# Kernel tuning notes

Hardware: AMD Instinct MI355X
Metric: run time of the kernel (lower is better)

The kernel has to match this reference:

```python
import jax, jax.numpy as jnp
import numpy as np

N = 6144      # nodes
DIN = 65      # input_dim (1 time + 64 space coords)
DOUT = 65     # output_dim per head
H = 4         # nheads
EPS = 1e-7
MIN = 1e-15
# curvature c = 1 throughout (MultiHeadGraphAttentionLayer hardcodes curvature=1)

def arcosh(z):
    return jnp.log(z + jnp.sqrt(jnp.maximum(z * z - 1.0, 0.0)))

def hyp_proj(u):
    # project onto hyperboloid: recompute time coord
    y = u[..., 1:]
    t = jnp.sqrt(1.0 + jnp.sum(y * y, -1, keepdims=True))
    return jnp.concatenate([t, y], -1)

def expmap0(u):
    v = u[..., 1:]
    n = jnp.maximum(jnp.linalg.norm(v, axis=-1, keepdims=True), MIN)
    return jnp.concatenate([jnp.cosh(n), jnp.sinh(n) * v / n], -1)

def logmap0(x):
    y = x[..., 1:]
    n = jnp.maximum(jnp.linalg.norm(y, axis=-1, keepdims=True), MIN)
    t = jnp.maximum(x[..., :1], 1.0 + EPS)
    return jnp.concatenate([jnp.zeros_like(t), arcosh(t) * y / n], -1)

def hyp_linear(x, W):
    # HypLinear (use_bias=False, eval mode): mobius_matvec = exp0(log0(x) @ W^T), then proj
    return hyp_proj(expmap0(logmap0(x) @ W.T))

def to_poincare(x):
    return x[..., 1:] / (x[..., :1] + 1.0)

def to_hyperboloid(p):
    s = jnp.sum(p * p, -1, keepdims=True)
    return jnp.concatenate([1.0 + s, 2.0 * p], -1) / jnp.maximum(1.0 - s, MIN)

def mobius_half(v):
    # 0.5 (x) v  (mobius scalar multiplication, c=1)
    n = jnp.maximum(jnp.linalg.norm(v, axis=-1, keepdims=True), MIN)
    return jnp.tanh(0.5 * jnp.arctanh(jnp.minimum(n, 1.0 - EPS))) * v / n

def head(x, adj_t, Wa, Wd, Wo):
    att = hyp_linear(x, Wa)   # [N, DOUT]
    red = hyp_linear(x, Wd)   # [N, DOUT]
    # pairwise hyperboloid sqdist via Minkowski inner product (negate time coord)
    am = att.at[:, 0].multiply(-1.0)
    theta = jnp.maximum(-(am @ att.T), 1.0 + EPS)          # [N, N]
    S = jnp.minimum(arcosh(theta) ** 2, 50.0)
    # coef[i, j] = -adj[j, i] * sqdist for incoming edges (mask = adj^T)
    coef = jnp.where(adj_t > 0.01, -adj_t * S, 0.0)
    # F.normalize along incoming-edge axis (zeros don't change the L2 norm)
    a = coef / jnp.maximum(jnp.linalg.norm(coef, axis=-1, keepdims=True), 1e-12)
    pv = to_poincare(red)                                   # [N, DOUT-1]
    lam = 2.0 / jnp.maximum(1.0 - jnp.sum(pv * pv, -1), MIN)  # conformal factors [N]
    num = (a * lam[None, :]) @ pv                           # [N, DOUT-1]
    den = jnp.sum(jnp.abs(a) * (lam - 1.0)[None, :], -1, keepdims=True)
    m = mobius_half(num / jnp.maximum(den, MIN))            # mobius midpoint
    return hyp_linear(to_hyperboloid(m), Wo)                # [N, DOUT]

def reference(x, adj, W_att, W_data, W_out, W_lin):
    adj_t = adj.T
    hs = jnp.stack([head(x, adj_t, W_att[h], W_data[h], W_out[h]) for h in range(H)], axis=1)  # [N, H, DOUT]
    p = to_poincare(hs).reshape(x.shape[0], -1)             # PoincareBall.concat -> [N, H*(DOUT-1)]
    return hyp_linear(to_hyperboloid(p), W_lin)             # [N, H*DOUT]

def setup_inputs():
    key = jax.random.key(0)
    ks = jax.random.split(key, 8)
    sp = 0.1 * jax.random.normal(ks[0], (N, DIN - 1), jnp.float32)
    x = jnp.concatenate([jnp.sqrt(1.0 + jnp.sum(sp * sp, -1, keepdims=True)), sp], -1)
    adj = (jax.random.uniform(ks[1], (N, N)) < 32.0 / N).astype(jnp.float32)
    adj = jnp.maximum(adj, jnp.eye(N, dtype=jnp.float32))  # every node >=1 incoming edge
    def xavier(k, shape):
        b = (6.0 / (shape[0] + shape[1])) ** 0.5
        return jax.random.uniform(k, shape, jnp.float32, -b, b)
    W_att = jnp.stack([xavier(jax.random.fold_in(ks[2], h), (DOUT, DIN)) for h in range(H)])
    W_data = jnp.stack([xavier(jax.random.fold_in(ks[3], h), (DOUT, DIN)) for h in range(H)])
    W_out = jnp.stack([xavier(jax.random.fold_in(ks[4], h), (DOUT, DOUT)) for h in range(H)])
    W_lin = xavier(ks[5], (H * DOUT, H * (DOUT - 1) + 1))
    return {"x": x, "adj": adj, "W_att": W_att, "W_data": W_data, "W_out": W_out, "W_lin": W_lin}
```

## Files before the change

### kernel.cpp

```cpp
#include <hip/hip_runtime.h>
#include <hip/hip_fp16.h>
#include <math.h>

#define N 6144
#define H 4
#define CAP 128
#define MINF 1e-15f
#define ONE_EPS  1.0000001192092896f
#define ONE_MEPS 0.9999998807907104f

__device__ __forceinline__ float wave_reduce_sum(float v) {
    v += __shfl_xor(v, 32, 64);
    v += __shfl_xor(v, 16, 64);
    v += __shfl_xor(v, 8, 64);
    v += __shfl_xor(v, 4, 64);
    v += __shfl_xor(v, 2, 64);
    v += __shfl_xor(v, 1, 64);
    return v;
}

__device__ __forceinline__ float arcosh_f(float z) {
    return logf(z + sqrtf(fmaxf(z * z - 1.0f, 0.0f)));
}

__device__ __forceinline__ void h8_to_f(float4 r, float* o) {
    __half2* h = (__half2*)&r;
    #pragma unroll
    for (int q = 0; q < 4; q++) {
        float2 f = __half22float2(h[q]);
        o[2 * q + 0] = f.x;
        o[2 * q + 1] = f.y;
    }
}

__device__ __forceinline__ int bitrev4(int t) {
    return ((t & 1) << 3) | ((t & 2) << 1) | ((t & 4) >> 1) | ((t & 8) >> 3);
}

__global__ void k_prep(const float* __restrict__ x, float* __restrict__ lmv,
                       const float* __restrict__ W_att, const float* __restrict__ W_data,
                       const float* __restrict__ W_out, const float* __restrict__ Wl,
                       float* __restrict__ Bp, float* __restrict__ Bo,
                       float* __restrict__ WlT, int* __restrict__ cnt) {
    int b = blockIdx.x;
    if (b < 1536) {
        int i = b * 4 + (threadIdx.x >> 6);
        int lane = threadIdx.x & 63;
        float y = x[i * 65 + 1 + lane];
        float ss = wave_reduce_sum(y * y);
        float n = fmaxf(sqrtf(ss), MINF);
        float t = fmaxf(x[i * 65], ONE_EPS);
        lmv[i * 64 + lane] = arcosh_f(t) * y / n;
    } else if (b < 1728) {
        int tid = (b - 1536) * 256 + threadIdx.x;
        int m = tid >> 12;
        int r = tid & 4095;
        int k = r >> 6, o = r & 63;
        const float* src;
        if (m < 4) src = W_att + m * 65 * 65;
        else if (m < 8) src = W_data + (m - 4) * 65 * 65;
        else src = W_out + (m - 8) * 65 * 65;
        if (m < 8) {
            Bp[m * 4096 + k * 64 + o] = src[(1 + o) * 65 + (1 + k)];
        } else {
            int dk = (k & 3) * 16 + bitrev4(k >> 2);
            Bo[(m - 8) * 4096 + k * 64 + o] = src[(1 + o) * 65 + (1 + dk)];
        }
    } else if (b < 1808) {
        int L = ((b - 1728) * 256 + threadIdx.x) * 4;
        int k = L / 320, o0 = L % 320;
        float v[4];
        #pragma unroll
        for (int q = 0; q < 4; q++) {
            int o = o0 + q;
            v[q] = (o < 259) ? Wl[(size_t)(1 + o) * 257 + 1 + k] : 0.f;
        }
        *(float4*)(WlT + L) = make_float4(v[0], v[1], v[2], v[3]);
    } else {
        cnt[(b - 1808) * 256 + threadIdx.x] = 0;
    }
}

__global__ void __launch_bounds__(256) k_csr_gemm(
        const float* __restrict__ adj, int* __restrict__ cnt, int* __restrict__ idx,
        const float* __restrict__ lmv, const float* __restrict__ Bp,
        __half* __restrict__ kv, float2* __restrict__ a0l) {
    __shared__ float smem[64 * 65];
    if (blockIdx.x < 768) {
        float (*As)[64] = (float(*)[64])smem;
        float (*Bs)[64] = (float(*)[64])(smem + 1024);
        float (*Cs)[65] = (float(*)[65])smem;
        int my = blockIdx.x / 96;
        int ix = blockIdx.x % 96;
        const float* Bb = Bp + (size_t)my * 4096;
        int i0 = ix * 64;
        int tid = threadIdx.x;
        int tx = tid & 15, ty = tid >> 4;
        float acc[4][4] = {};
        for (int k0 = 0; k0 < 64; k0 += 16) {
            {
                int mm = tid >> 2, kq = tid & 3;
                float4 v = *(const float4*)(lmv + (size_t)(i0 + mm) * 64 + k0 + kq * 4);
                As[kq * 4 + 0][mm] = v.x;
                As[kq * 4 + 1][mm] = v.y;
                As[kq * 4 + 2][mm] = v.z;
                As[kq * 4 + 3][mm] = v.w;
            }
            {
                int kk = tid >> 4, o4 = tid & 15;
                float4 bvv = *(const float4*)(Bb + (k0 + kk) * 64 + o4 * 4);
                *(float4*)&Bs[kk][o4 * 4] = bvv;
            }
            __syncthreads();
            #pragma unroll
            for (int kk = 0; kk < 16; kk++) {
                float4 av = *(const float4*)&As[kk][ty * 4];
                float4 bv = *(const float4*)&Bs[kk][tx * 4];
                float a[4] = {av.x, av.y, av.z, av.w};
                float b[4] = {bv.x, bv.y, bv.z, bv.w};
                #pragma unroll
                for (int r = 0; r < 4; r++)
                    #pragma unroll
                    for (int c = 0; c < 4; c++) acc[r][c] += a[r] * b[c];
            }
            __syncthreads();
        }
        #pragma unroll
        for (int r = 0; r < 4; r++)
            #pragma unroll
            for (int c = 0; c < 4; c++)
                Cs[ty * 4 + r][tx * 4 + c] = acc[r][c];
        __syncthreads();
        int w = tid >> 6, lane = tid & 63;
        bool isAtt = my < 4;
        int h = my & 3;
        #pragma unroll 1
        for (int r = 0; r < 16; r++) {
            int row = w * 16 + r;
            int i = i0 + row;
            float u = Cs[row][lane];
            float nn = fmaxf(sqrtf(wave_reduce_sum(u * u)), MINF);
            if (isAtt) {
                float sha = sinhf(nn);
                kv[((size_t)h * N + i) * 128 + lane] = __float2half(sha * u / nn);
                if (lane == 0) a0l[h * N + i].x = coshf(nn);
            } else {
                float shd = sinhf(nn), chd = coshf(nn);
                float pvd = (shd * u / nn) / (chd + 1.0f);
                kv[((size_t)h * N + i) * 128 + 64 + lane] = __float2half(pvd);
                float sp = wave_reduce_sum(pvd * pvd);
                if (lane == 0) a0l[h * N + i].y = 2.0f / fmaxf(1.0f - sp, MINF);
            }
        }
    } else {
        const float4* a4 = (const float4*)adj;
        const unsigned STRIDE = 1048576u;
        unsigned e0 = (blockIdx.x - 768) * 256 + threadIdx.x;
        float4 v0 = a4[e0];
        float4 v1 = a4[e0 + STRIDE];
        #pragma unroll 1
        for (int it = 0; it < 9; it++) {
            float4 vn;
            if (it < 7) vn = a4[e0 + (unsigned)(it + 2) * STRIDE];
            unsigned base = (e0 + (unsigned)it * STRIDE) * 4u;
            float vals[4] = {v0.x, v0.y, v0.z, v0.w};
            #pragma unroll
            for (int q = 0; q < 4; q++) {
                if (vals[q] > 0.01f) {
                    unsigned t = base + q;
                    int j = t / N;
                    int i = t % N;
                    int pos = atomicAdd(&cnt[i], 1);
                    if (pos < CAP) idx[i * CAP + pos] = j;
                }
            }
            v0 = v1;
            v1 = vn;
        }
    }
}

__global__ void __launch_bounds__(256) k_attn(
        const int* __restrict__ cnt, const int* __restrict__ idx,
        const __half* __restrict__ kv, const float2* __restrict__ a0l,
        float* __restrict__ lm2) {
    int w = threadIdx.x >> 6, lane = threadIdx.x & 63;
    int gb = blockIdx.x;
    int slot = gb & 7;
    int h = slot >> 1;
    int iblk = (gb >> 3) * 2 + (slot & 1);
    int i = iblk * 4 + w;

    const __half* kvh = kv + (size_t)h * N * 128;
    const float2* a0lh = a0l + (size_t)h * N;
    int c = lane & 3, t = lane >> 2;

    float ai[16];
    {
        float4 r0 = *(const float4*)(kvh + (size_t)i * 128 + c * 16);
        float4 r1 = *(const float4*)(kvh + (size_t)i * 128 + c * 16 + 8);
        h8_to_f(r0, ai);
        h8_to_f(r1, ai + 8);
    }
    float ai0 = a0lh[i].x;
    int nn = min(cnt[i], CAP);

    float accd = 0.f, accss = 0.f;
    float accn16[16] = {};
    for (int base = 0; base < nn; base += 16) {
        int tt = base + t;
        bool act = tt < nn;
        int j = act ? idx[i * CAP + tt] : i;
        float2 al = a0lh[j];
        const __half* row = kvh + (size_t)j * 128;
        float4 b0 = *(const float4*)(row + c * 16);
        float4 b1 = *(const float4*)(row + c * 16 + 8);
        float4 p0 = *(const float4*)(row + 64 + c * 16);
        float4 p1 = *(const float4*)(row + 64 + c * 16 + 8);
        float bv[16], pw[16];
        h8_to_f(b0, bv);
        h8_to_f(b1, bv + 8);
        h8_to_f(p0, pw);
        h8_to_f(p1, pw + 8);
        float d = 0.f;
        #pragma unroll
        for (int k = 0; k < 16; k++) d += ai[k] * bv[k];
        d += __shfl_xor(d, 1, 64);
        d += __shfl_xor(d, 2, 64);
        float theta = fmaxf(ai0 * al.x - d, ONE_EPS);
        float ar = arcosh_f(theta);
        float S = fminf(ar * ar, 50.0f);
        if (!act || j == i) S = 0.f;
        float wq = S * al.y;
        if (c == 0) {
            accd += S * (al.y - 1.0f);
            accss += S * S;
        }
        #pragma unroll
        for (int k = 0; k < 16; k++) accn16[k] = fmaf(wq, pw[k], accn16[k]);
    }
    accd = wave_reduce_sum(accd);
    accss = wave_reduce_sum(accss);
    float nrm = fmaxf(sqrtf(accss), 1e-12f);
    float den = fmaxf(accd / nrm, MINF);
    float scl = 1.0f / (nrm * den);

    float r8[8];
    {
        bool b0 = t & 1;
        #pragma unroll
        for (int kk = 0; kk < 8; kk++) {
            float mine = b0 ? accn16[kk + 8] : accn16[kk];
            float send = b0 ? accn16[kk] : accn16[kk + 8];
            r8[kk] = mine + __shfl_xor(send, 4, 64);
        }
    }
    float r4[4];
    {
        bool b1 = t & 2;
        #pragma unroll
        for (int kk = 0; kk < 4; kk++) {
            float mine = b1 ? r8[kk + 4] : r8[kk];
            float send = b1 ? r8[kk] : r8[kk + 4];
            r4[kk] = mine + __shfl_xor(send, 8, 64);
        }
    }
    float r2[2];
    {
        bool b2 = t & 4;
        #pragma unroll
        for (int kk = 0; kk < 2; kk++) {
            float mine = b2 ? r4[kk + 2] : r4[kk];
            float send = b2 ? r4[kk] : r4[kk + 2];
            r2[kk] = mine + __shfl_xor(send, 16, 64);
        }
    }
    float r1;
    {
        bool b3 = t & 8;
        float mine = b3 ? r2[1] : r2[0];
        float send = b3 ? r2[0] : r2[1];
        r1 = mine + __shfl_xor(send, 32, 64);
    }

    float v = -scl * r1;
    float nv = fmaxf(sqrtf(wave_reduce_sum(v * v)), MINF);
    float nc = fminf(nv, ONE_MEPS);
    float mh = tanhf(0.5f * atanhf(nc));
    float md = mh * v / nv;
    float s = wave_reduce_sum(md * md);
    float Dh = fmaxf(1.0f - s, MINF);
    float hb0 = (1.0f + s) / Dh;
    float hbv = 2.0f * md / Dh;
    float nh = fmaxf(2.0f * sqrtf(s) / Dh, MINF);
    float t2 = fmaxf(hb0, ONE_EPS);
    lm2[((size_t)h * N + i) * 64 + lane] = arcosh_f(t2) * hbv / nh;
}

#define PS 272
#define BS5 336
__global__ void __launch_bounds__(256) k_tail(
        const float* __restrict__ lm2, const float* __restrict__ Bo,
        const float* __restrict__ WlT, float* __restrict__ out) {
    __shared__ float smem[5376 + 16 * PS];
    float* As1 = smem;
    float* Bs1 = smem + 1088;
    float* Bs5 = smem;
    float* P   = smem + 5376;

    int i0 = blockIdx.x * 16;
    int tid = threadIdx.x;
    int ty = tid >> 4;
    int tx = tid & 15;

    for (int h = 0; h < H; h++) {
        {
            float4 v = *(const float4*)(lm2 + ((size_t)h * N + i0 + ty) * 64 + tx * 4);
            *(float4*)(As1 + ty * 68 + tx * 4) = v;
        }
        float acc[4] = {0.f, 0.f, 0.f, 0.f};
        for (int k0 = 0; k0 < 64; k0 += 16) {
            {
                *(float4*)(Bs1 + ty * 64 + tx * 4) =
                    *(const float4*)(Bo + (size_t)h * 4096 + (k0 + ty) * 64 + tx * 4);
            }
            __syncthreads();
            #pragma unroll
            for (int kk = 0; kk < 16; kk++) {
                float a = As1[ty * 68 + k0 + kk];
                float4 bv = *(const float4*)(Bs1 + kk * 64 + tx * 4);
                acc[0] += a * bv.x;
                acc[1] += a * bv.y;
                acc[2] += a * bv.z;
                acc[3] += a * bv.w;
            }
            __syncthreads();
        }
        float ss = acc[0] * acc[0] + acc[1] * acc[1] + acc[2] * acc[2] + acc[3] * acc[3];
        ss += __shfl_xor(ss, 1, 64);
        ss += __shfl_xor(ss, 2, 64);
        ss += __shfl_xor(ss, 4, 64);
        ss += __shfl_xor(ss, 8, 64);
        float nn = fmaxf(sqrtf(ss), MINF);
        float sh = sinhf(nn), ch = coshf(nn);
        float* Pr = P + ty * PS + h * 64 + tx * 4;
        Pr[0] = (sh * acc[0] / nn) / (ch + 1.0f);
        Pr[1] = (sh * acc[1] / nn) / (ch + 1.0f);
        Pr[2] = (sh * acc[2] / nn) / (ch + 1.0f);
        Pr[3] = (sh * acc[3] / nn) / (ch + 1.0f);
    }
    __syncthreads();

    {
        float sp = 0.f;
        float4 pl[4];
        #pragma unroll
        for (int q = 0; q < 4; q++) {
            pl[q] = *(const float4*)(P + ty * PS + q * 64 + tx * 4);
            sp += pl[q].x * pl[q].x + pl[q].y * pl[q].y
                + pl[q].z * pl[q].z + pl[q].w * pl[q].w;
        }
        sp += __shfl_xor(sp, 1, 64);
        sp += __shfl_xor(sp, 2, 64);
        sp += __shfl_xor(sp, 4, 64);
        sp += __shfl_xor(sp, 8, 64);
        float Dh = fmaxf(1.0f - sp, MINF);
        float t2 = fmaxf((1.0f + sp) / Dh, ONE_EPS);
        float nh = fmaxf(2.0f * sqrtf(sp) / Dh, MINF);
        float ar2 = arcosh_f(t2);
        #pragma unroll
        for (int q = 0; q < 4; q++) {
            float4 v = pl[q];
            v.x = ar2 * (2.0f * v.x / Dh) / nh;
            v.y = ar2 * (2.0f * v.y / Dh) / nh;
            v.z = ar2 * (2.0f * v.z / Dh) / nh;
            v.w = ar2 * (2.0f * v.w / Dh) / nh;
            *(float4*)(P + ty * PS + q * 64 + tx * 4) = v;
        }
    }
    __syncthreads();

    float acc2[5][4] = {};
    for (int k0 = 0; k0 < 256; k0 += 16) {
        {
            #pragma unroll
            for (int q = 0; q < 5; q++)
                *(float4*)(Bs5 + ty * BS5 + q * 64 + tx * 4) =
                    *(const float4*)(WlT + (size_t)(k0 + ty) * 320 + q * 64 + tx * 4);
        }
        __syncthreads();
        #pragma unroll
        for (int kq = 0; kq < 4; kq++) {
            float4 pv4 = *(const float4*)(P + ty * PS + k0 + kq * 4);
            float av[4] = {pv4.x, pv4.y, pv4.z, pv4.w};
            #pragma unroll
            for (int j = 0; j < 4; j++) {
                float a = av[j];
                int kk = kq * 4 + j;
                #pragma unroll
                for (int q = 0; q < 5; q++) {
                    float4 bv = *(const float4*)(Bs5 + kk * BS5 + q * 64 + tx * 4);
                    acc2[q][0] += a * bv.x;
                    acc2[q][1] += a * bv.y;
                    acc2[q][2] += a * bv.z;
                    acc2[q][3] += a * bv.w;
                }
            }
        }
        __syncthreads();
    }

    float ss2 = 0.f;
    #pragma unroll
    for (int q = 0; q < 5; q++)
        ss2 += acc2[q][0] * acc2[q][0] + acc2[q][1] * acc2[q][1]
             + acc2[q][2] * acc2[q][2] + acc2[q][3] * acc2[q][3];
    ss2 += __shfl_xor(ss2, 1, 64);
    ss2 += __shfl_xor(ss2, 2, 64);
    ss2 += __shfl_xor(ss2, 4, 64);
    ss2 += __shfl_xor(ss2, 8, 64);
    float nv = fmaxf(sqrtf(ss2), MINF);
    float sh2 = sinhf(nv);
    float scale = sh2 / nv;
    size_t ob = (size_t)(i0 + ty) * 260;
    #pragma unroll
    for (int q = 0; q < 4; q++) {
        int o = q * 64 + tx * 4;
        out[ob + 1 + o + 0] = scale * acc2[q][0];
        out[ob + 1 + o + 1] = scale * acc2[q][1];
        out[ob + 1 + o + 2] = scale * acc2[q][2];
        out[ob + 1 + o + 3] = scale * acc2[q][3];
    }
    if (tx == 0) {
        out[ob] = sqrtf(1.0f + sh2 * sh2);
        out[ob + 257] = scale * acc2[4][0];
        out[ob + 258] = scale * acc2[4][1];
        out[ob + 259] = scale * acc2[4][2];
    }
}

extern "C" void kernel_launch(void* const* d_in, const int* in_sizes, int n_in,
                              void* d_out, int out_size, void* d_ws, size_t ws_size,
                              hipStream_t stream) {
    const float* x = (const float*)d_in[0];
    const float* adj = (const float*)d_in[1];
    const float* W_att = (const float*)d_in[2];
    const float* W_data = (const float*)d_in[3];
    const float* W_out = (const float*)d_in[4];
    const float* W_lin = (const float*)d_in[5];
    float* out = (float*)d_out;

    char* ws = (char*)d_ws;
    size_t off = 0;
    auto alloc = [&](size_t bytes) {
        void* ptr = ws + off;
        off += (bytes + 255) & ~(size_t)255;
        return ptr;
    };
    int* cnt = (int*)alloc((size_t)N * 4);
    int* idx = (int*)alloc((size_t)N * CAP * 4);
    float* lmv = (float*)alloc((size_t)N * 64 * 4);
    __half* kv = (__half*)alloc((size_t)H * N * 128 * 2);
    float2* a0l = (float2*)alloc((size_t)H * N * 8);
    float* lm2 = (float*)alloc((size_t)H * N * 64 * 4);
    float* Bp = (float*)alloc((size_t)8 * 4096 * 4);
    float* Bo = (float*)alloc((size_t)4 * 4096 * 4);
    float* WlT = (float*)alloc((size_t)256 * 320 * 4);

    k_prep<<<1832, 256, 0, stream>>>(x, lmv, W_att, W_data, W_out, W_lin,
                                     Bp, Bo, WlT, cnt);
    k_csr_gemm<<<4864, 256, 0, stream>>>(adj, cnt, idx, lmv, Bp, kv, a0l);
    k_attn<<<6144, 256, 0, stream>>>(cnt, idx, kv, a0l, lm2);
    k_tail<<<N / 16, 256, 0, stream>>>(lm2, Bo, WlT, out);
}
```

Before: 313.9 us.

## Fuse all stages into one cooperative persistent kernel with grid syncs

```diff
diff --git a/kernel.cpp b/kernel.cpp
--- a/kernel.cpp
+++ b/kernel.cpp
@@ -1,6 +1,9 @@
 #include <hip/hip_runtime.h>
 #include <hip/hip_fp16.h>
+#include <hip/hip_cooperative_groups.h>
 #include <math.h>
+
+namespace cg = cooperative_groups;
 
 #define N 6144
 #define H 4
@@ -8,6 +11,7 @@
 #define MINF 1e-15f
 #define ONE_EPS  1.0000001192092896f
 #define ONE_MEPS 0.9999998807907104f
+#define NBLK 1024
 
 __device__ __forceinline__ float wave_reduce_sum(float v) {
     v += __shfl_xor(v, 32, 64);
@@ -37,24 +41,26 @@
     return ((t & 1) << 3) | ((t & 2) << 1) | ((t & 4) >> 1) | ((t & 8) >> 3);
 }
 
-__global__ void k_prep(const float* __restrict__ x, float* __restrict__ lmv,
-                       const float* __restrict__ W_att, const float* __restrict__ W_data,
-                       const float* __restrict__ W_out, const float* __restrict__ Wl,
-                       float* __restrict__ Bp, float* __restrict__ Bo,
-                       float* __restrict__ WlT, int* __restrict__ cnt) {
-    int b = blockIdx.x;
+
+__device__ __forceinline__ void prep_unit(
+        int b, int tid,
+        const float* __restrict__ x, float* __restrict__ lmv,
+        const float* __restrict__ W_att, const float* __restrict__ W_data,
+        const float* __restrict__ W_out, const float* __restrict__ Wl,
+        float* __restrict__ Bp, float* __restrict__ Bo,
+        float* __restrict__ WlT, int* __restrict__ cnt) {
     if (b < 1536) {
-        int i = b * 4 + (threadIdx.x >> 6);
-        int lane = threadIdx.x & 63;
+        int i = b * 4 + (tid >> 6);
+        int lane = tid & 63;
         float y = x[i * 65 + 1 + lane];
         float ss = wave_reduce_sum(y * y);
         float n = fmaxf(sqrtf(ss), MINF);
         float t = fmaxf(x[i * 65], ONE_EPS);
         lmv[i * 64 + lane] = arcosh_f(t) * y / n;
     } else if (b < 1728) {
-        int tid = (b - 1536) * 256 + threadIdx.x;
-        int m = tid >> 12;
-        int r = tid & 4095;
+        int t = (b - 1536) * 256 + tid;
+        int m = t >> 12;
+        int r = t & 4095;
         int k = r >> 6, o = r & 63;
         const float* src;
         if (m < 4) src = W_att + m * 65 * 65;
@@ -67,7 +73,7 @@
             Bo[(m - 8) * 4096 + k * 64 + o] = src[(1 + o) * 65 + (1 + dk)];
         }
     } else if (b < 1808) {
-        int L = ((b - 1728) * 256 + threadIdx.x) * 4;
+        int L = ((b - 1728) * 256 + tid) * 4;
         int k = L / 320, o0 = L % 320;
         float v[4];
         #pragma unroll
@@ -77,120 +83,108 @@
         }
         *(float4*)(WlT + L) = make_float4(v[0], v[1], v[2], v[3]);
     } else {
-        cnt[(b - 1808) * 256 + threadIdx.x] = 0;
-    }
-}
-
-__global__ void __launch_bounds__(256) k_csr_gemm(
-        const float* __restrict__ adj, int* __restrict__ cnt, int* __restrict__ idx,
+        cnt[(b - 1808) * 256 + tid] = 0;
+    }
+}
+
+__device__ __forceinline__ void scan_adj(
+        const float4* __restrict__ a4, int* __restrict__ cnt,
+        int* __restrict__ idx, unsigned e0, unsigned stride, int iters) {
+    float4 v0 = a4[e0];
+    #pragma unroll 1
+    for (int it = 0; it < iters; it++) {
+        float4 vn;
+        if (it + 1 < iters) vn = a4[e0 + (unsigned)(it + 1) * stride];
+        unsigned base = (e0 + (unsigned)it * stride) * 4u;
+        float vals[4] = {v0.x, v0.y, v0.z, v0.w};
+        #pragma unroll
+        for (int q = 0; q < 4; q++) {
+            if (vals[q] > 0.01f) {
+                unsigned t = base + q;
+                int j = t / N;
+                int i = t % N;
+                int pos = atomicAdd(&cnt[i], 1);
+                if (pos < CAP) idx[i * CAP + pos] = j;
+            }
+        }
+        v0 = vn;
+    }
+}
+
+__device__ __forceinline__ void gemm1_tile(
+        int my, int ix, int tid, float* smem,
         const float* __restrict__ lmv, const float* __restrict__ Bp,
         __half* __restrict__ kv, float2* __restrict__ a0l) {
-    __shared__ float smem[64 * 65];
-    if (blockIdx.x < 768) {
-        float (*As)[64] = (float(*)[64])smem;
-        float (*Bs)[64] = (float(*)[64])(smem + 1024);
-        float (*Cs)[65] = (float(*)[65])smem;
-        int my = blockIdx.x / 96;
-        int ix = blockIdx.x % 96;
-        const float* Bb = Bp + (size_t)my * 4096;
-        int i0 = ix * 64;
-        int tid = threadIdx.x;
-        int tx = tid & 15, ty = tid >> 4;
-        float acc[4][4] = {};
-        for (int k0 = 0; k0 < 64; k0 += 16) {
-            {
-                int mm = tid >> 2, kq = tid & 3;
-                float4 v = *(const float4*)(lmv + (size_t)(i0 + mm) * 64 + k0 + kq * 4);
-                As[kq * 4 + 0][mm] = v.x;
-                As[kq * 4 + 1][mm] = v.y;
-                As[kq * 4 + 2][mm] = v.z;
-                As[kq * 4 + 3][mm] = v.w;
-            }
-            {
-                int kk = tid >> 4, o4 = tid & 15;
-                float4 bvv = *(const float4*)(Bb + (k0 + kk) * 64 + o4 * 4);
-                *(float4*)&Bs[kk][o4 * 4] = bvv;
-            }
-            __syncthreads();
+    float (*As)[64] = (float(*)[64])smem;
+    float (*Bs)[64] = (float(*)[64])(smem + 1024);
+    float (*Cs)[65] = (float(*)[65])smem;
+    const float* Bb = Bp + (size_t)my * 4096;
+    int i0 = ix * 64;
+    int tx = tid & 15, ty = tid >> 4;
+    float acc[4][4] = {};
+    for (int k0 = 0; k0 < 64; k0 += 16) {
+        {
+            int mm = tid >> 2, kq = tid & 3;
+            float4 v = *(const float4*)(lmv + (size_t)(i0 + mm) * 64 + k0 + kq * 4);
+            As[kq * 4 + 0][mm] = v.x;
+            As[kq * 4 + 1][mm] = v.y;
+            As[kq * 4 + 2][mm] = v.z;
+            As[kq * 4 + 3][mm] = v.w;
+        }
+        {
+            int kk = tid >> 4, o4 = tid & 15;
+            float4 bvv = *(const float4*)(Bb + (k0 + kk) * 64 + o4 * 4);
+            *(float4*)&Bs[kk][o4 * 4] = bvv;
+        }
+        __syncthreads();
+        #pragma unroll
+        for (int kk = 0; kk < 16; kk++) {
+            float4 av = *(const float4*)&As[kk][ty * 4];
+            float4 bv = *(const float4*)&Bs[kk][tx * 4];
+            float a[4] = {av.x, av.y, av.z, av.w};
+            float b[4] = {bv.x, bv.y, bv.z, bv.w};
             #pragma unroll
-            for (int kk = 0; kk < 16; kk++) {
-                float4 av = *(const float4*)&As[kk][ty * 4];
-                float4 bv = *(const float4*)&Bs[kk][tx * 4];
-                float a[4] = {av.x, av.y, av.z, av.w};
-                float b[4] = {bv.x, bv.y, bv.z, bv.w};
+            for (int r = 0; r < 4; r++)
                 #pragma unroll
-                for (int r = 0; r < 4; r++)
-                    #pragma unroll
-                    for (int c = 0; c < 4; c++) acc[r][c] += a[r] * b[c];
-            }
-            __syncthreads();
-        }
-        #pragma unroll
-        for (int r = 0; r < 4; r++)
-            #pragma unroll
-            for (int c = 0; c < 4; c++)
-                Cs[ty * 4 + r][tx * 4 + c] = acc[r][c];
+                for (int c = 0; c < 4; c++) acc[r][c] += a[r] * b[c];
+        }
         __syncthreads();
-        int w = tid >> 6, lane = tid & 63;
-        bool isAtt = my < 4;
-        int h = my & 3;
-        #pragma unroll 1
-        for (int r = 0; r < 16; r++) {
-            int row = w * 16 + r;
-            int i = i0 + row;
-            float u = Cs[row][lane];
-            float nn = fmaxf(sqrtf(wave_reduce_sum(u * u)), MINF);
-            if (isAtt) {
-                float sha = sinhf(nn);
-                kv[((size_t)h * N + i) * 128 + lane] = __float2half(sha * u / nn);
-                if (lane == 0) a0l[h * N + i].x = coshf(nn);
-            } else {
-                float shd = sinhf(nn), chd = coshf(nn);
-                float pvd = (shd * u / nn) / (chd + 1.0f);
-                kv[((size_t)h * N + i) * 128 + 64 + lane] = __float2half(pvd);
-                float sp = wave_reduce_sum(pvd * pvd);
-                if (lane == 0) a0l[h * N + i].y = 2.0f / fmaxf(1.0f - sp, MINF);
-            }
-        }
-    } else {
-        const float4* a4 = (const float4*)adj;
-        const unsigned STRIDE = 1048576u;
-        unsigned e0 = (blockIdx.x - 768) * 256 + threadIdx.x;
-        float4 v0 = a4[e0];
-        float4 v1 = a4[e0 + STRIDE];
-        #pragma unroll 1
-        for (int it = 0; it < 9; it++) {
-            float4 vn;
-            if (it < 7) vn = a4[e0 + (unsigned)(it + 2) * STRIDE];
-            unsigned base = (e0 + (unsigned)it * STRIDE) * 4u;
-            float vals[4] = {v0.x, v0.y, v0.z, v0.w};
-            #pragma unroll
-            for (int q = 0; q < 4; q++) {
-                if (vals[q] > 0.01f) {
-                    unsigned t = base + q;
-                    int j = t / N;
-                    int i = t % N;
-                    int pos = atomicAdd(&cnt[i], 1);
-                    if (pos < CAP) idx[i * CAP + pos] = j;
-                }
-            }
-            v0 = v1;
-            v1 = vn;
-        }
-    }
-}
-
-__global__ void __launch_bounds__(256) k_attn(
+    }
+    #pragma unroll
+    for (int r = 0; r < 4; r++)
+        #pragma unroll
+        for (int c = 0; c < 4; c++)
+            Cs[ty * 4 + r][tx * 4 + c] = acc[r][c];
+    __syncthreads();
+    int w = tid >> 6, lane = tid & 63;
+    bool isAtt = my < 4;
+    int h = my & 3;
+    #pragma unroll 1
+    for (int r = 0; r < 16; r++) {
+        int row = w * 16 + r;
+        int i = i0 + row;
+        float u = Cs[row][lane];
+        float nn = fmaxf(sqrtf(wave_reduce_sum(u * u)), MINF);
+        if (isAtt) {
+            float sha = sinhf(nn);
+            kv[((size_t)h * N + i) * 128 + lane] = __float2half(sha * u / nn);
+            if (lane == 0) a0l[h * N + i].x = coshf(nn);
+        } else {
+            float shd = sinhf(nn), chd = coshf(nn);
+            float pvd = (shd * u / nn) / (chd + 1.0f);
+            kv[((size_t)h * N + i) * 128 + 64 + lane] = __float2half(pvd);
+            float sp = wave_reduce_sum(pvd * pvd);
+            if (lane == 0) a0l[h * N + i].y = 2.0f / fmaxf(1.0f - sp, MINF);
+        }
+    }
+    __syncthreads();
+}
+
+__device__ __forceinline__ void attn_unit(
+        int i, int h, int lane,
         const int* __restrict__ cnt, const int* __restrict__ idx,
         const __half* __restrict__ kv, const float2* __restrict__ a0l,
         float* __restrict__ lm2) {
-    int w = threadIdx.x >> 6, lane = threadIdx.x & 63;
-    int gb = blockIdx.x;
-    int slot = gb & 7;
-    int h = slot >> 1;
-    int iblk = (gb >> 3) * 2 + (slot & 1);
-    int i = iblk * 4 + w;
-
     const __half* kvh = kv + (size_t)h * N * 128;
     const float2* a0lh = a0l + (size_t)h * N;
     int c = lane & 3, t = lane >> 2;
@@ -299,17 +293,14 @@
 
 #define PS 272
 #define BS5 336
-__global__ void __launch_bounds__(256) k_tail(
+__device__ __forceinline__ void tail_tile(
+        int i0, int tid, float* smem,
         const float* __restrict__ lm2, const float* __restrict__ Bo,
         const float* __restrict__ WlT, float* __restrict__ out) {
-    __shared__ float smem[5376 + 16 * PS];
     float* As1 = smem;
     float* Bs1 = smem + 1088;
     float* Bs5 = smem;
     float* P   = smem + 5376;
-
-    int i0 = blockIdx.x * 16;
-    int tid = threadIdx.x;
     int ty = tid >> 4;
     int tx = tid & 15;
 
@@ -439,6 +430,91 @@
     }
 }
 
+__global__ void __launch_bounds__(256, 4) k_mega(
+        const float* __restrict__ x, const float* __restrict__ adj,
+        const float* __restrict__ W_att, const float* __restrict__ W_data,
+        const float* __restrict__ W_out, const float* __restrict__ Wl,
+        float* __restrict__ lmv, float* __restrict__ Bp, float* __restrict__ Bo,
+        float* __restrict__ WlT, int* __restrict__ cnt, int* __restrict__ idx,
+        __half* __restrict__ kv, float2* __restrict__ a0l,
+        float* __restrict__ lm2, float* __restrict__ out) {
+    cg::grid_group grid = cg::this_grid();
+    __shared__ float smem[9728];
+    int bid = blockIdx.x, tid = threadIdx.x;
+
+    for (int u = bid; u < 1832; u += NBLK)
+        prep_unit(u, tid, x, lmv, W_att, W_data, W_out, Wl, Bp, Bo, WlT, cnt);
+    grid.sync();
+
+    if (bid < 768) {
+        gemm1_tile(bid / 96, bid % 96, tid, smem, lmv, Bp, kv, a0l);
+        scan_adj((const float4*)adj, cnt, idx,
+                 (unsigned)(bid * 256 + tid), 196608u, 34);
+    } else {
+        scan_adj((const float4*)adj, cnt, idx,
+                 6684672u + (unsigned)((bid - 768) * 256 + tid), 65536u, 42);
+    }
+    grid.sync();
+
+    {
+        int w = tid >> 6, lane = tid & 63;
+        int slot = bid & 7;
+        int h = slot >> 1;
+        int ih = (bid >> 3) * 2 + (slot & 1);
+        #pragma unroll 1
+        for (int it = 0; it < 6; it++) {
+            int ublk = it * 256 + ih;
+            attn_unit(ublk * 4 + w, h, lane, cnt, idx, kv, a0l, lm2);
+        }
+    }
+    grid.sync();
+
+    if (bid < 384)
+        tail_tile(bid * 16, tid, smem, lm2, Bo, WlT, out);
+}
+
+__global__ void k_prep(const float* __restrict__ x, float* __restrict__ lmv,
+                       const float* __restrict__ W_att, const float* __restrict__ W_data,
+                       const float* __restrict__ W_out, const float* __restrict__ Wl,
+                       float* __restrict__ Bp, float* __restrict__ Bo,
+                       float* __restrict__ WlT, int* __restrict__ cnt) {
+    prep_unit(blockIdx.x, threadIdx.x, x, lmv, W_att, W_data, W_out, Wl,
+              Bp, Bo, WlT, cnt);
+}
+
+__global__ void __launch_bounds__(256) k_csr_gemm(
+        const float* __restrict__ adj, int* __restrict__ cnt, int* __restrict__ idx,
+        const float* __restrict__ lmv, const float* __restrict__ Bp,
+        __half* __restrict__ kv, float2* __restrict__ a0l) {
+    __shared__ float smem[64 * 65];
+    if (blockIdx.x < 768) {
+        gemm1_tile(blockIdx.x / 96, blockIdx.x % 96, threadIdx.x, smem,
+                   lmv, Bp, kv, a0l);
+    } else {
+        scan_adj((const float4*)adj, cnt, idx,
+                 (unsigned)((blockIdx.x - 768) * 256 + threadIdx.x), 1048576u, 9);
+    }
+}
+
+__global__ void __launch_bounds__(256) k_attn(
+        const int* __restrict__ cnt, const int* __restrict__ idx,
+        const __half* __restrict__ kv, const float2* __restrict__ a0l,
+        float* __restrict__ lm2) {
+    int w = threadIdx.x >> 6, lane = threadIdx.x & 63;
+    int gb = blockIdx.x;
+    int slot = gb & 7;
+    int h = slot >> 1;
+    int iblk = (gb >> 3) * 2 + (slot & 1);
+    attn_unit(iblk * 4 + w, h, lane, cnt, idx, kv, a0l, lm2);
+}
+
+__global__ void __launch_bounds__(256) k_tail(
+        const float* __restrict__ lm2, const float* __restrict__ Bo,
+        const float* __restrict__ WlT, float* __restrict__ out) {
+    __shared__ float smem[9728];
+    tail_tile(blockIdx.x * 16, threadIdx.x, smem, lm2, Bo, WlT, out);
+}
+
 extern "C" void kernel_launch(void* const* d_in, const int* in_sizes, int n_in,
                               void* d_out, int out_size, void* d_ws, size_t ws_size,
                               hipStream_t stream) {
@@ -467,9 +543,18 @@
     float* Bo = (float*)alloc((size_t)4 * 4096 * 4);
     float* WlT = (float*)alloc((size_t)256 * 320 * 4);
 
-    k_prep<<<1832, 256, 0, stream>>>(x, lmv, W_att, W_data, W_out, W_lin,
-                                     Bp, Bo, WlT, cnt);
-    k_csr_gemm<<<4864, 256, 0, stream>>>(adj, cnt, idx, lmv, Bp, kv, a0l);
-    k_attn<<<6144, 256, 0, stream>>>(cnt, idx, kv, a0l, lm2);
-    k_tail<<<N / 16, 256, 0, stream>>>(lm2, Bo, WlT, out);
-}
+    void* args[] = {(void*)&x, (void*)&adj, (void*)&W_att, (void*)&W_data,
+                    (void*)&W_out, (void*)&W_lin, (void*)&lmv, (void*)&Bp,
+                    (void*)&Bo, (void*)&WlT, (void*)&cnt, (void*)&idx,
+                    (void*)&kv, (void*)&a0l, (void*)&lm2, (void*)&out};
+    hipError_t err = hipLaunchCooperativeKernel(
+        reinterpret_cast<void*>(k_mega), dim3(NBLK), dim3(256), args, 0, stream);
+    if (err != hipSuccess) {
+        (void)hipGetLastError();
+        k_prep<<<1832, 256, 0, stream>>>(x, lmv, W_att, W_data, W_out, W_lin,
+                                         Bp, Bo, WlT, cnt);
+        k_csr_gemm<<<4864, 256, 0, stream>>>(adj, cnt, idx, lmv, Bp, kv, a0l);
+        k_attn<<<6144, 256, 0, stream>>>(cnt, idx, kv, a0l, lm2);
+        k_tail<<<N / 16, 256, 0, stream>>>(lm2, Bo, WlT, out);
+    }
+}
```

Measured after the change: 693.4 us. 121% more time.

## Fold prep kernel into CSR/GEMM kernel, compute logmap0 and weight transposes in-place

Applied to the files above, without the earlier changes.

```diff
diff --git a/kernel.cpp b/kernel.cpp
--- a/kernel.cpp
+++ b/kernel.cpp
@@ -37,85 +37,59 @@
     return ((t & 1) << 3) | ((t & 2) << 1) | ((t & 4) >> 1) | ((t & 8) >> 3);
 }
 
-__global__ void k_prep(const float* __restrict__ x, float* __restrict__ lmv,
-                       const float* __restrict__ W_att, const float* __restrict__ W_data,
-                       const float* __restrict__ W_out, const float* __restrict__ Wl,
-                       float* __restrict__ Bp, float* __restrict__ Bo,
-                       float* __restrict__ WlT, int* __restrict__ cnt) {
-    int b = blockIdx.x;
-    if (b < 1536) {
-        int i = b * 4 + (threadIdx.x >> 6);
-        int lane = threadIdx.x & 63;
-        float y = x[i * 65 + 1 + lane];
-        float ss = wave_reduce_sum(y * y);
-        float n = fmaxf(sqrtf(ss), MINF);
-        float t = fmaxf(x[i * 65], ONE_EPS);
-        lmv[i * 64 + lane] = arcosh_f(t) * y / n;
-    } else if (b < 1728) {
-        int tid = (b - 1536) * 256 + threadIdx.x;
-        int m = tid >> 12;
-        int r = tid & 4095;
-        int k = r >> 6, o = r & 63;
-        const float* src;
-        if (m < 4) src = W_att + m * 65 * 65;
-        else if (m < 8) src = W_data + (m - 4) * 65 * 65;
-        else src = W_out + (m - 8) * 65 * 65;
-        if (m < 8) {
-            Bp[m * 4096 + k * 64 + o] = src[(1 + o) * 65 + (1 + k)];
-        } else {
-            int dk = (k & 3) * 16 + bitrev4(k >> 2);
-            Bo[(m - 8) * 4096 + k * 64 + o] = src[(1 + o) * 65 + (1 + dk)];
-        }
-    } else if (b < 1808) {
-        int L = ((b - 1728) * 256 + threadIdx.x) * 4;
-        int k = L / 320, o0 = L % 320;
-        float v[4];
-        #pragma unroll
-        for (int q = 0; q < 4; q++) {
-            int o = o0 + q;
-            v[q] = (o < 259) ? Wl[(size_t)(1 + o) * 257 + 1 + k] : 0.f;
-        }
-        *(float4*)(WlT + L) = make_float4(v[0], v[1], v[2], v[3]);
-    } else {
-        cnt[(b - 1808) * 256 + threadIdx.x] = 0;
-    }
+__global__ void k_zero(int* __restrict__ cnt) {
+    cnt[blockIdx.x * 1024 + threadIdx.x] = 0;
 }
 
 __global__ void __launch_bounds__(256) k_csr_gemm(
         const float* __restrict__ adj, int* __restrict__ cnt, int* __restrict__ idx,
-        const float* __restrict__ lmv, const float* __restrict__ Bp,
+        const float* __restrict__ x,
+        const float* __restrict__ W_att, const float* __restrict__ W_data,
+        const float* __restrict__ W_out, const float* __restrict__ Wl,
+        float* __restrict__ Bo, float* __restrict__ WlT,
         __half* __restrict__ kv, float2* __restrict__ a0l) {
-    __shared__ float smem[64 * 65];
+    __shared__ float smem[5376];
     if (blockIdx.x < 768) {
-        float (*As)[64] = (float(*)[64])smem;
-        float (*Bs)[64] = (float(*)[64])(smem + 1024);
+        float* Bs = smem;
+        float* At = smem + 1024;
         float (*Cs)[65] = (float(*)[65])smem;
         int my = blockIdx.x / 96;
         int ix = blockIdx.x % 96;
-        const float* Bb = Bp + (size_t)my * 4096;
+        const float* Wsrc = (my < 4) ? (W_att + my * 4225)
+                                     : (W_data + (my - 4) * 4225);
         int i0 = ix * 64;
         int tid = threadIdx.x;
         int tx = tid & 15, ty = tid >> 4;
+        int w = tid >> 6, lane = tid & 63;
+
+        #pragma unroll 1
+        for (int r8 = 0; r8 < 16; r8++) {
+            int row = w * 16 + r8;
+            int i = i0 + row;
+            float y = x[i * 65 + 1 + lane];
+            float ss = wave_reduce_sum(y * y);
+            float n = fmaxf(sqrtf(ss), MINF);
+            float t = fmaxf(x[i * 65], ONE_EPS);
+            At[lane * 68 + row] = arcosh_f(t) * y / n;
+        }
+        __syncthreads();
+
         float acc[4][4] = {};
         for (int k0 = 0; k0 < 64; k0 += 16) {
             {
-                int mm = tid >> 2, kq = tid & 3;
-                float4 v = *(const float4*)(lmv + (size_t)(i0 + mm) * 64 + k0 + kq * 4);
-                As[kq * 4 + 0][mm] = v.x;
-                As[kq * 4 + 1][mm] = v.y;
-                As[kq * 4 + 2][mm] = v.z;
-                As[kq * 4 + 3][mm] = v.w;
-            }
-            {
                 int kk = tid >> 4, o4 = tid & 15;
-                float4 bvv = *(const float4*)(Bb + (k0 + kk) * 64 + o4 * 4);
-                *(float4*)&Bs[kk][o4 * 4] = bvv;
+                int col = 1 + k0 + kk;
+                float b0 = Wsrc[(1 + o4 * 4 + 0) * 65 + col];
+                float b1 = Wsrc[(1 + o4 * 4 + 1) * 65 + col];
+                float b2 = Wsrc[(1 + o4 * 4 + 2) * 65 + col];
+                float b3 = Wsrc[(1 + o4 * 4 + 3) * 65 + col];
+                *(float4*)&Bs[kk * 64 + o4 * 4] = make_float4(b0, b1, b2, b3);
             }
             __syncthreads();
             #pragma unroll
             for (int kk = 0; kk < 16; kk++) {
-                float4 av = *(const float4*)&As[kk][ty * 4];
-                float4 bv = *(const float4*)&Bs[kk][tx * 4];
+                float4 av = *(const float4*)&At[(k0 + kk) * 68 + ty * 4];
+                float4 bv = *(const float4*)&Bs[kk * 64 + tx * 4];
                 float a[4] = {av.x, av.y, av.z, av.w};
                 float b[4] = {bv.x, bv.y, bv.z, bv.w};
                 #pragma unroll
@@ -131,7 +105,6 @@
             for (int c = 0; c < 4; c++)
                 Cs[ty * 4 + r][tx * 4 + c] = acc[r][c];
         __syncthreads();
-        int w = tid >> 6, lane = tid & 63;
         bool isAtt = my < 4;
         int h = my & 3;
         #pragma unroll 1
@@ -153,9 +126,28 @@
             }
         }
     } else {
+        int sb = blockIdx.x - 768;
+        if (sb < 64) {
+            int t = sb * 256 + threadIdx.x;
+            int m2 = t >> 12;
+            int r = t & 4095;
+            int k = r >> 6, o = r & 63;
+            int dk = (k & 3) * 16 + bitrev4(k >> 2);
+            Bo[m2 * 4096 + k * 64 + o] = W_out[m2 * 4225 + (1 + o) * 65 + (1 + dk)];
+        } else if (sb < 144) {
+            int L = ((sb - 64) * 256 + threadIdx.x) * 4;
+            int k = L / 320, o0 = L % 320;
+            float v[4];
+            #pragma unroll
+            for (int q = 0; q < 4; q++) {
+                int o = o0 + q;
+                v[q] = (o < 259) ? Wl[(size_t)(1 + o) * 257 + 1 + k] : 0.f;
+            }
+            *(float4*)(WlT + L) = make_float4(v[0], v[1], v[2], v[3]);
+        }
         const float4* a4 = (const float4*)adj;
         const unsigned STRIDE = 1048576u;
-        unsigned e0 = (blockIdx.x - 768) * 256 + threadIdx.x;
+        unsigned e0 = (unsigned)sb * 256 + threadIdx.x;
         float4 v0 = a4[e0];
         float4 v1 = a4[e0 + STRIDE];
         #pragma unroll 1
@@ -459,17 +451,15 @@
     };
     int* cnt = (int*)alloc((size_t)N * 4);
     int* idx = (int*)alloc((size_t)N * CAP * 4);
-    float* lmv = (float*)alloc((size_t)N * 64 * 4);
     __half* kv = (__half*)alloc((size_t)H * N * 128 * 2);
     float2* a0l = (float2*)alloc((size_t)H * N * 8);
     float* lm2 = (float*)alloc((size_t)H * N * 64 * 4);
-    float* Bp = (float*)alloc((size_t)8 * 4096 * 4);
     float* Bo = (float*)alloc((size_t)4 * 4096 * 4);
     float* WlT = (float*)alloc((size_t)256 * 320 * 4);
 
-    k_prep<<<1832, 256, 0, stream>>>(x, lmv, W_att, W_data, W_out, W_lin,
-                                     Bp, Bo, WlT, cnt);
-    k_csr_gemm<<<4864, 256, 0, stream>>>(adj, cnt, idx, lmv, Bp, kv, a0l);
+    k_zero<<<6, 1024, 0, stream>>>(cnt);
+    k_csr_gemm<<<4864, 256, 0, stream>>>(adj, cnt, idx, x, W_att, W_data,
+                                         W_out, W_lin, Bo, WlT, kv, a0l);
     k_attn<<<6144, 256, 0, stream>>>(cnt, idx, kv, a0l, lm2);
     k_tail<<<N / 16, 256, 0, stream>>>(lm2, Bo, WlT, out);
 }
```

After: 335.0 us. 1.07x slower.
